# Optimization experiments

Hardware: AMD Instinct MI355X
Metric: run time of the kernel (lower is better)

## Reference

```python
import jax, jax.numpy as jnp
import numpy as np

N_NODES = 100000
N_EDGES = 3200000
EPS = 1e-5


def spmm(row, col, vals, h, n):
    # out[i] = sum_{e: row[e]==i} vals[e] * h[col[e]]  -- sparse A @ h in COO form
    return jax.ops.segment_sum(vals[:, None] * h[col], row, num_segments=n)


def batchnorm(h, gamma, beta):
    # BatchNorm1d in training mode: biased batch statistics over the node dim
    mean = jnp.mean(h, axis=0)
    var = jnp.mean((h - mean) ** 2, axis=0)
    return (h - mean) * jax.lax.rsqrt(var + EPS) * gamma + beta


def setup_inputs() -> dict:
    key = jax.random.key(0)
    ks = jax.random.split(key, 8)
    x = jax.random.normal(ks[0], (N_NODES, 256), dtype=jnp.float32)
    vals = jax.random.uniform(ks[1], (N_EDGES,), dtype=jnp.float32)
    row = jax.random.randint(ks[2], (N_EDGES,), 0, N_NODES, dtype=jnp.int32)
    col = jax.random.randint(ks[3], (N_EDGES,), 0, N_NODES, dtype=jnp.int32)
    W0 = jax.random.normal(ks[4], (256, 256), dtype=jnp.float32) * 0.05
    W1 = jax.random.normal(ks[5], (256, 256), dtype=jnp.float32) * 0.05
    W2 = jax.random.normal(ks[6], (256, 128), dtype=jnp.float32) * 0.05
    b0 = jnp.zeros((256,), jnp.float32)
    b1 = jnp.zeros((256,), jnp.float32)
    b2 = jnp.zeros((128,), jnp.float32)
    g0 = jnp.ones((256,), jnp.float32)
    g1 = jnp.ones((256,), jnp.float32)
    be0 = jnp.zeros((256,), jnp.float32)
    be1 = jnp.zeros((256,), jnp.float32)
    return {"x": x, "vals": vals, "W0": W0, "b0": b0, "g0": g0, "be0": be0,
            "W1": W1, "b1": b1, "g1": g1, "be1": be1, "W2": W2, "b2": b2,
            "row": row, "col": col}


def reference(x, vals, W0, b0, g0, be0, W1, b1, g1, be1, W2, b2, row, col):
    n = x.shape[0]
    # layer 0: linear -> SpMM -> BN -> ReLU (dropout is identity in eval)
    h = spmm(row, col, vals, x @ W0 + b0, n)
    h = jax.nn.relu(batchnorm(h, g0, be0))
    # layer 1
    h = spmm(row, col, vals, h @ W1 + b1, n)
    h = jax.nn.relu(batchnorm(h, g1, be1))
    # final projection
    h = spmm(row, col, vals, h @ W2 + b2, n)
    return h
```

## Files before the change

### kernel.cpp

```cpp
#include <hip/hip_runtime.h>


typedef __attribute__((ext_vector_type(8))) short s8b;
typedef __attribute__((ext_vector_type(4))) float f32x4;

__device__ inline unsigned short bf16_rne(float f) {
    unsigned u = __float_as_uint(f);
    return (unsigned short)((u + 0x7fffu + ((u >> 16) & 1u)) >> 16);
}
__device__ inline float bf16_to_f(unsigned short h) {
    return __uint_as_float((unsigned)h << 16);
}

#define NBLK_AC 256

__global__ __launch_bounds__(256) void bucket_hist(const int* __restrict__ row,
                                                   int* __restrict__ hist2d,
                                                   int E, int NB) {
    __shared__ int cnt[256];
    int t = threadIdx.x, blk = blockIdx.x;
    cnt[t] = 0;
    __syncthreads();
    int chunk = (E + gridDim.x - 1) / gridDim.x;
    int e0 = blk * chunk, e1 = min(E, e0 + chunk);
    for (int e = e0 + t; e < e1; e += 256) atomicAdd(&cnt[((unsigned)row[e]) >> 9], 1);
    __syncthreads();
    if (t < NB) hist2d[t * NBLK_AC + blk] = cnt[t];
}

__global__ __launch_bounds__(1024) void excl_scan(const int* __restrict__ in,
                                                  int* __restrict__ out, int L) {
    __shared__ int wsum[16];
    __shared__ int s_run;
    int t = threadIdx.x;
    int wid = t >> 6, lane = t & 63;
    if (t == 0) s_run = 0;
    __syncthreads();
    const int CHUNK = 1024 * 8;
    for (int base = 0; base < L; base += CHUNK) {
        int v[8];
        int local = 0;
        int i0 = base + t * 8;
#pragma unroll
        for (int j = 0; j < 8; ++j) {
            int idx = i0 + j;
            v[j] = (idx < L) ? in[idx] : 0;
            local += v[j];
        }
        int x = local;
#pragma unroll
        for (int off = 1; off < 64; off <<= 1) {
            int y = __shfl_up(x, off);
            if (lane >= off) x += y;
        }
        if (lane == 63) wsum[wid] = x;
        __syncthreads();
        if (wid == 0) {
            int w = (lane < 16) ? wsum[lane] : 0;
#pragma unroll
            for (int off = 1; off < 16; off <<= 1) {
                int y = __shfl_up(w, off);
                if (lane >= off) w += y;
            }
            if (lane < 16) wsum[lane] = w;
        }
        __syncthreads();
        int wave_off = (wid > 0) ? wsum[wid - 1] : 0;
        int chunk_total = wsum[15];
        int acc = (x - local) + wave_off + s_run;
#pragma unroll
        for (int j = 0; j < 8; ++j) {
            int idx = i0 + j;
            if (idx < L) out[idx] = acc;
            acc += v[j];
        }
        __syncthreads();
        if (t == 0) s_run += chunk_total;
        __syncthreads();
    }
}

__global__ __launch_bounds__(256) void bucket_scatter(const int* __restrict__ row,
                                                      const int* __restrict__ col,
                                                      const float* __restrict__ vals,
                                                      const int* __restrict__ base2d,
                                                      int2* __restrict__ ebuf,
                                                      int E, int NB) {
    __shared__ int cur[256];
    int t = threadIdx.x, blk = blockIdx.x;
    if (t < NB) cur[t] = base2d[t * NBLK_AC + blk];
    __syncthreads();
    int chunk = (E + gridDim.x - 1) / gridDim.x;
    int e0 = blk * chunk, e1 = min(E, e0 + chunk);
    for (int e = e0 + t; e < e1; e += 256) {
        int r = row[e];
        int b = ((unsigned)r) >> 9;
        int p = atomicAdd(&cur[b], 1);
        ebuf[p] = make_int2(((r & 511) << 23) | col[e], __float_as_int(vals[e]));
    }
}

__global__ __launch_bounds__(256) void bucket_sort(const int2* __restrict__ ebuf,
                                                   const int* __restrict__ base2d,
                                                   int2* __restrict__ edges,
                                                   int* __restrict__ rowptr,
                                                   int E, int M, int NB) {
    __shared__ int cnt[512];
    __shared__ int excl[512];
    int b = blockIdx.x, t = threadIdx.x;
    int bstart = base2d[b * NBLK_AC];
    int bend = (b + 1 < NB) ? base2d[(b + 1) * NBLK_AC] : E;
    cnt[t] = 0;
    cnt[t + 256] = 0;
    __syncthreads();
    for (int i = bstart + t; i < bend; i += 256)
        atomicAdd(&cnt[((unsigned)ebuf[i].x) >> 23], 1);
    __syncthreads();
    if (t == 0) {
        int a = 0;
#pragma unroll 8
        for (int i = 0; i < 512; ++i) { excl[i] = a; a += cnt[i]; }
    }
    __syncthreads();
    for (int rl = t; rl < 512; rl += 256) {
        int r0 = b * 512 + rl;
        if (r0 < M) rowptr[r0] = bstart + excl[rl];
    }
    if (b == 0 && t == 0) rowptr[M] = E;
    cnt[t] = excl[t];
    cnt[t + 256] = excl[t + 256];
    __syncthreads();
    for (int i = bstart + t; i < bend; i += 256) {
        int2 eb = ebuf[i];
        int rl = ((unsigned)eb.x) >> 23;
        int p = bstart + atomicAdd(&cnt[rl], 1);
        edges[p] = make_int2(eb.x & 0x7FFFFF, eb.y);
    }
}

__global__ void wsplit_kernel(const float* __restrict__ W, short* __restrict__ Wt_hi,
                              short* __restrict__ Wt_lo, int N) {
    const int K = 256;
    int i = blockIdx.x * blockDim.x + threadIdx.x;
    if (i >= K * N) return;
    int k = i / N, n = i % N;
    float f = W[i];
    unsigned short h = bf16_rne(f);
    unsigned short l = bf16_rne(f - bf16_to_f(h));
    Wt_hi[(size_t)n * K + k] = (short)h;
    Wt_lo[(size_t)n * K + k] = (short)l;
}

template <bool FIRST>
__global__ __launch_bounds__(256) void gemm_mfma_kernel(
    const void* __restrict__ Aptr, const short* __restrict__ Wth,
    const short* __restrict__ Wtl, const float* __restrict__ bias,
    const float* __restrict__ scale, const float* __restrict__ shift,
    unsigned short* __restrict__ C, int M, int N) {
    const int K = 256;
    const int LDT = 40;
    __shared__ short Ah[128 * LDT], Bh[128 * LDT], Bl[128 * LDT];

    int t = threadIdx.x;
    int wave = t >> 6, lane = t & 63;
    int wm = wave >> 1, wn = wave & 1;
    int row0 = blockIdx.x * 128;
    int n0 = blockIdx.y * 128;

    int srow = t >> 1;
    int skh = (t & 1) * 16;

    int lr = lane & 15;
    int lg = (lane >> 4) * 8;

    f32x4 acc[4][4];
#pragma unroll
    for (int i = 0; i < 4; ++i)
#pragma unroll
        for (int j = 0; j < 4; ++j) acc[i][j] = (f32x4){0.f, 0.f, 0.f, 0.f};

    for (int k0 = 0; k0 < K; k0 += 32) {
        float va[16];
        int gr = row0 + srow;
        if constexpr (FIRST) {
            if (gr < M) {
                const float4* ap = (const float4*)((const float*)Aptr + (size_t)gr * K + k0 + skh);
#pragma unroll
                for (int q = 0; q < 4; ++q) {
                    float4 v = ap[q];
                    va[4 * q + 0] = v.x; va[4 * q + 1] = v.y;
                    va[4 * q + 2] = v.z; va[4 * q + 3] = v.w;
                }
            } else {
#pragma unroll
                for (int q = 0; q < 16; ++q) va[q] = 0.f;
            }
        } else {
            if (gr < M) {
                const s8b* ap = (const s8b*)((const unsigned short*)Aptr + (size_t)gr * K + k0 + skh);
                s8b r0 = ap[0], r1 = ap[1];
#pragma unroll
                for (int q = 0; q < 8; ++q) {
                    va[q] = bf16_to_f((unsigned short)r0[q]);
                    va[8 + q] = bf16_to_f((unsigned short)r1[q]);
                }
            } else {
#pragma unroll
                for (int q = 0; q < 16; ++q) va[q] = 0.f;
            }
#pragma unroll
            for (int q = 0; q < 4; ++q) {
                float4 sc = *(const float4*)(scale + k0 + skh + 4 * q);
                float4 sh = *(const float4*)(shift + k0 + skh + 4 * q);
                va[4 * q + 0] = fmaxf(va[4 * q + 0] * sc.x + sh.x, 0.f);
                va[4 * q + 1] = fmaxf(va[4 * q + 1] * sc.y + sh.y, 0.f);
                va[4 * q + 2] = fmaxf(va[4 * q + 2] * sc.z + sh.z, 0.f);
                va[4 * q + 3] = fmaxf(va[4 * q + 3] * sc.w + sh.w, 0.f);
            }
        }
        s8b vh0, vh1;
#pragma unroll
        for (int q = 0; q < 8; ++q) {
            vh0[q] = (short)bf16_rne(va[q]);
            vh1[q] = (short)bf16_rne(va[8 + q]);
        }
        *(s8b*)&Ah[srow * LDT + skh]     = vh0;
        *(s8b*)&Ah[srow * LDT + skh + 8] = vh1;

        int gn = n0 + srow;
        const s8b* wph = (const s8b*)(Wth + (size_t)gn * K + k0 + skh);
        const s8b* wpl = (const s8b*)(Wtl + (size_t)gn * K + k0 + skh);
        s8b wh0 = wph[0], wh1 = wph[1];
        s8b wl0 = wpl[0], wl1 = wpl[1];
        *(s8b*)&Bh[srow * LDT + skh]     = wh0;
        *(s8b*)&Bh[srow * LDT + skh + 8] = wh1;
        *(s8b*)&Bl[srow * LDT + skh]     = wl0;
        *(s8b*)&Bl[srow * LDT + skh + 8] = wl1;
        __syncthreads();

        s8b a[4], bh[4], bl[4];
#pragma unroll
        for (int i = 0; i < 4; ++i)
            a[i] = *(const s8b*)&Ah[(wm * 64 + i * 16 + lr) * LDT + lg];
#pragma unroll
        for (int j = 0; j < 4; ++j) {
            int c = (wn * 64 + j * 16 + lr) * LDT + lg;
            bh[j] = *(const s8b*)&Bh[c];
            bl[j] = *(const s8b*)&Bl[c];
        }
#pragma unroll
        for (int i = 0; i < 4; ++i)
#pragma unroll
            for (int j = 0; j < 4; ++j) {
                acc[i][j] = __builtin_amdgcn_mfma_f32_16x16x32_bf16(a[i], bh[j], acc[i][j], 0, 0, 0);
                acc[i][j] = __builtin_amdgcn_mfma_f32_16x16x32_bf16(a[i], bl[j], acc[i][j], 0, 0, 0);
            }
        __syncthreads();
    }

    int lq = lane >> 4;
#pragma unroll
    for (int j = 0; j < 4; ++j) {
        int colg = n0 + wn * 64 + j * 16 + lr;
        float bb = bias[colg];
#pragma unroll
        for (int i = 0; i < 4; ++i) {
#pragma unroll
            for (int r = 0; r < 4; ++r) {
                int rowg = row0 + wm * 64 + i * 16 + lq * 4 + r;
                if (rowg < M) C[(size_t)rowg * N + colg] = bf16_rne(acc[i][j][r] + bb);
            }
        }
    }
}

template <int F, bool OUT_BF16>
__global__ __launch_bounds__(256) void spmm_kernel(const int* __restrict__ rowptr,
                                                   const int2* __restrict__ edges,
                                                   const unsigned short* __restrict__ H,
                                                   void* __restrict__ out, int M) {
    int wid = threadIdx.x >> 6;
    int lane = threadIdx.x & 63;
    int r = blockIdx.x * 4 + wid;
    if (r >= M) return;
    int e0 = rowptr[r], e1 = rowptr[r + 1];
    if constexpr (F == 256) {
        const ushort4* Hv = (const ushort4*)H;
        float4 acc = {0.f, 0.f, 0.f, 0.f};
        int e = e0;
        for (; e + 4 <= e1; e += 4) {
            int2 E0 = edges[e], E1 = edges[e + 1], E2 = edges[e + 2], E3 = edges[e + 3];
            ushort4 h0 = Hv[(size_t)E0.x * 64 + lane];
            ushort4 h1 = Hv[(size_t)E1.x * 64 + lane];
            ushort4 h2 = Hv[(size_t)E2.x * 64 + lane];
            ushort4 h3 = Hv[(size_t)E3.x * 64 + lane];
            float v0 = __int_as_float(E0.y), v1 = __int_as_float(E1.y);
            float v2 = __int_as_float(E2.y), v3 = __int_as_float(E3.y);
            acc.x += v0 * bf16_to_f(h0.x); acc.y += v0 * bf16_to_f(h0.y);
            acc.z += v0 * bf16_to_f(h0.z); acc.w += v0 * bf16_to_f(h0.w);
            acc.x += v1 * bf16_to_f(h1.x); acc.y += v1 * bf16_to_f(h1.y);
            acc.z += v1 * bf16_to_f(h1.z); acc.w += v1 * bf16_to_f(h1.w);
            acc.x += v2 * bf16_to_f(h2.x); acc.y += v2 * bf16_to_f(h2.y);
            acc.z += v2 * bf16_to_f(h2.z); acc.w += v2 * bf16_to_f(h2.w);
            acc.x += v3 * bf16_to_f(h3.x); acc.y += v3 * bf16_to_f(h3.y);
            acc.z += v3 * bf16_to_f(h3.z); acc.w += v3 * bf16_to_f(h3.w);
        }
        for (; e < e1; ++e) {
            int2 E0 = edges[e];
            ushort4 h0 = Hv[(size_t)E0.x * 64 + lane];
            float v0 = __int_as_float(E0.y);
            acc.x += v0 * bf16_to_f(h0.x); acc.y += v0 * bf16_to_f(h0.y);
            acc.z += v0 * bf16_to_f(h0.z); acc.w += v0 * bf16_to_f(h0.w);
        }
        if constexpr (OUT_BF16) {
            ushort4 o;
            o.x = bf16_rne(acc.x); o.y = bf16_rne(acc.y);
            o.z = bf16_rne(acc.z); o.w = bf16_rne(acc.w);
            ((ushort4*)out)[(size_t)r * 64 + lane] = o;
        } else {
            ((float4*)out)[(size_t)r * 64 + lane] = acc;
        }
    } else {
        const ushort2* Hv = (const ushort2*)H;
        float2 acc = {0.f, 0.f};
        int e = e0;
        for (; e + 4 <= e1; e += 4) {
            int2 E0 = edges[e], E1 = edges[e + 1], E2 = edges[e + 2], E3 = edges[e + 3];
            ushort2 h0 = Hv[(size_t)E0.x * 64 + lane];
            ushort2 h1 = Hv[(size_t)E1.x * 64 + lane];
            ushort2 h2 = Hv[(size_t)E2.x * 64 + lane];
            ushort2 h3 = Hv[(size_t)E3.x * 64 + lane];
            float v0 = __int_as_float(E0.y), v1 = __int_as_float(E1.y);
            float v2 = __int_as_float(E2.y), v3 = __int_as_float(E3.y);
            acc.x += v0 * bf16_to_f(h0.x); acc.y += v0 * bf16_to_f(h0.y);
            acc.x += v1 * bf16_to_f(h1.x); acc.y += v1 * bf16_to_f(h1.y);
            acc.x += v2 * bf16_to_f(h2.x); acc.y += v2 * bf16_to_f(h2.y);
            acc.x += v3 * bf16_to_f(h3.x); acc.y += v3 * bf16_to_f(h3.y);
        }
        for (; e < e1; ++e) {
            int2 E0 = edges[e];
            ushort2 h0 = Hv[(size_t)E0.x * 64 + lane];
            float v0 = __int_as_float(E0.y);
            acc.x += v0 * bf16_to_f(h0.x); acc.y += v0 * bf16_to_f(h0.y);
        }
        if constexpr (OUT_BF16) {
            ushort2 o;
            o.x = bf16_rne(acc.x); o.y = bf16_rne(acc.y);
            ((ushort2*)out)[(size_t)r * 64 + lane] = o;
        } else {
            ((float2*)out)[(size_t)r * 64 + lane] = acc;
        }
    }
}

__global__ __launch_bounds__(256) void bn_stats_kernel(const unsigned short* __restrict__ H,
                                                       float* __restrict__ sums,
                                                       float* __restrict__ sumsq, int M) {
    int c = threadIdx.x;
    int nb = gridDim.x;
    int rows_per = (M + nb - 1) / nb;
    int r0 = blockIdx.x * rows_per;
    int r1 = min(M, r0 + rows_per);
    float s = 0.f, q = 0.f;
    for (int r = r0; r < r1; ++r) {
        float v = bf16_to_f(H[(size_t)r * 256 + c]);
        s += v;
        q += v * v;
    }
    atomicAdd(&sums[c], s);
    atomicAdd(&sumsq[c], q);
}

__global__ void bn_finalize_kernel(const float* __restrict__ sums, const float* __restrict__ sumsq,
                                   const float* __restrict__ g, const float* __restrict__ be,
                                   float* __restrict__ scale, float* __restrict__ shift, int M) {
    int c = threadIdx.x;
    float mean = sums[c] / (float)M;
    float var = sumsq[c] / (float)M - mean * mean;
    float inv = rsqrtf(var + 1e-5f);
    float s = g[c] * inv;
    scale[c] = s;
    shift[c] = be[c] - mean * s;
}

extern "C" void kernel_launch(void* const* d_in, const int* in_sizes, int n_in,
                              void* d_out, int out_size, void* d_ws, size_t ws_size,
                              hipStream_t stream) {
    const float* x   = (const float*)d_in[0];
    const float* vals= (const float*)d_in[1];
    const float* W0  = (const float*)d_in[2];
    const float* b0  = (const float*)d_in[3];
    const float* g0  = (const float*)d_in[4];
    const float* be0 = (const float*)d_in[5];
    const float* W1  = (const float*)d_in[6];
    const float* b1  = (const float*)d_in[7];
    const float* g1  = (const float*)d_in[8];
    const float* be1 = (const float*)d_in[9];
    const float* W2  = (const float*)d_in[10];
    const float* b2  = (const float*)d_in[11];
    const int* row   = (const int*)d_in[12];
    const int* col   = (const int*)d_in[13];
    const int E = in_sizes[1];
    const int M = in_sizes[0] / 256;
    float* out = (float*)d_out;

    char* ws = (char*)d_ws;
    size_t off = 0;
    auto alloc = [&](size_t bytes) -> void* {
        void* p = ws + off;
        off += (bytes + 255) & ~(size_t)255;
        return p;
    };
    unsigned short* hA = (unsigned short*)alloc((size_t)M * 256 * 2);
    unsigned short* hB = (unsigned short*)alloc((size_t)M * 256 * 2);
    int2*  edges = (int2*)alloc((size_t)E * 8);
    int2*  ebuf  = (int2*)alloc((size_t)E * 8);
    int*   rowptr= (int*)alloc((size_t)(M + 1) * 4);
    float* sums  = (float*)alloc(256 * 4);
    float* sumsq = (float*)alloc(256 * 4);
    float* scale = (float*)alloc(256 * 4);
    float* shift = (float*)alloc(256 * 4);
    short* Wth   = (short*)alloc((size_t)256 * 256 * 2);
    short* Wtl   = (short*)alloc((size_t)256 * 256 * 2);
    const int NB = (M + 511) >> 9;
    int* hist2d = (int*)alloc((size_t)NB * NBLK_AC * 4);
    int* base2d = (int*)alloc((size_t)NB * NBLK_AC * 4);

    bucket_hist<<<NBLK_AC, 256, 0, stream>>>(row, hist2d, E, NB);
    excl_scan<<<1, 1024, 0, stream>>>(hist2d, base2d, NB * NBLK_AC);
    bucket_scatter<<<NBLK_AC, 256, 0, stream>>>(row, col, vals, base2d, ebuf, E, NB);
    bucket_sort<<<NB, 256, 0, stream>>>(ebuf, base2d, edges, rowptr, E, M, NB);

    int gx = (M + 127) / 128;
    int spmm_grid = (M + 3) / 4;

    wsplit_kernel<<<(256 * 256 + 255) / 256, 256, 0, stream>>>(W0, Wth, Wtl, 256);
    gemm_mfma_kernel<true><<<dim3(gx, 2), 256, 0, stream>>>(x, Wth, Wtl, b0, nullptr, nullptr, hA, M, 256);
    spmm_kernel<256, true><<<spmm_grid, 256, 0, stream>>>(rowptr, edges, hA, hB, M);

    hipMemsetAsync(sums, 0, 2048, stream);
    bn_stats_kernel<<<256, 256, 0, stream>>>(hB, sums, sumsq, M);
    bn_finalize_kernel<<<1, 256, 0, stream>>>(sums, sumsq, g0, be0, scale, shift, M);

    wsplit_kernel<<<(256 * 256 + 255) / 256, 256, 0, stream>>>(W1, Wth, Wtl, 256);
    gemm_mfma_kernel<false><<<dim3(gx, 2), 256, 0, stream>>>(hB, Wth, Wtl, b1, scale, shift, hA, M, 256);
    spmm_kernel<256, true><<<spmm_grid, 256, 0, stream>>>(rowptr, edges, hA, hB, M);

    hipMemsetAsync(sums, 0, 2048, stream);
    bn_stats_kernel<<<256, 256, 0, stream>>>(hB, sums, sumsq, M);
    bn_finalize_kernel<<<1, 256, 0, stream>>>(sums, sumsq, g1, be1, scale, shift, M);

    wsplit_kernel<<<(256 * 128 + 255) / 256, 256, 0, stream>>>(W2, Wth, Wtl, 128);
    gemm_mfma_kernel<false><<<dim3(gx, 1), 256, 0, stream>>>(hB, Wth, Wtl, b2, scale, shift, hA, M, 128);
    spmm_kernel<128, false><<<spmm_grid, 256, 0, stream>>>(rowptr, edges, hA, out, M);
}
```

Baseline: 1.321 ms.

## Drop LDS staging in GEMM; load MFMA fragments directly and unfuse BN-ReLU

The GEMM no longer stages A and W tiles through shared memory with barriers. Each wave now loads its MFMA operand fragments straight from global memory, converting fp32 input to bf16 in registers. The BatchNorm scale/shift plus ReLU that was fused into the GEMM A-load moves to a separate elementwise kernel writing a new bf16 buffer. This removes LDS traffic and syncs, but adds redundant global loads across waves and an extra read/write pass over the activation per layer.

```diff
diff --git a/kernel.cpp b/kernel.cpp
--- a/kernel.cpp
+++ b/kernel.cpp
@@ -151,25 +151,44 @@
     Wt_lo[(size_t)n * K + k] = (short)l;
 }
 
+__global__ __launch_bounds__(256) void act_kernel(const unsigned short* __restrict__ hB,
+                                                  const float* __restrict__ scale,
+                                                  const float* __restrict__ shift,
+                                                  unsigned short* __restrict__ hC,
+                                                  int n8) {
+    int i = blockIdx.x * blockDim.x + threadIdx.x;
+    int stride = gridDim.x * blockDim.x;
+    for (; i < n8; i += stride) {
+        int kb = (i & 31) * 8;
+        s8b h = ((const s8b*)hB)[i];
+        float4 s0 = *(const float4*)(scale + kb);
+        float4 s1 = *(const float4*)(scale + kb + 4);
+        float4 t0 = *(const float4*)(shift + kb);
+        float4 t1 = *(const float4*)(shift + kb + 4);
+        s8b o;
+        o[0] = (short)bf16_rne(fmaxf(bf16_to_f((unsigned short)h[0]) * s0.x + t0.x, 0.f));
+        o[1] = (short)bf16_rne(fmaxf(bf16_to_f((unsigned short)h[1]) * s0.y + t0.y, 0.f));
+        o[2] = (short)bf16_rne(fmaxf(bf16_to_f((unsigned short)h[2]) * s0.z + t0.z, 0.f));
+        o[3] = (short)bf16_rne(fmaxf(bf16_to_f((unsigned short)h[3]) * s0.w + t0.w, 0.f));
+        o[4] = (short)bf16_rne(fmaxf(bf16_to_f((unsigned short)h[4]) * s1.x + t1.x, 0.f));
+        o[5] = (short)bf16_rne(fmaxf(bf16_to_f((unsigned short)h[5]) * s1.y + t1.y, 0.f));
+        o[6] = (short)bf16_rne(fmaxf(bf16_to_f((unsigned short)h[6]) * s1.z + t1.z, 0.f));
+        o[7] = (short)bf16_rne(fmaxf(bf16_to_f((unsigned short)h[7]) * s1.w + t1.w, 0.f));
+        ((s8b*)hC)[i] = o;
+    }
+}
+
 template <bool FIRST>
-__global__ __launch_bounds__(256) void gemm_mfma_kernel(
+__global__ __launch_bounds__(256) void gemm_direct(
     const void* __restrict__ Aptr, const short* __restrict__ Wth,
     const short* __restrict__ Wtl, const float* __restrict__ bias,
-    const float* __restrict__ scale, const float* __restrict__ shift,
     unsigned short* __restrict__ C, int M, int N) {
     const int K = 256;
-    const int LDT = 40;
-    __shared__ short Ah[128 * LDT], Bh[128 * LDT], Bl[128 * LDT];
-
     int t = threadIdx.x;
     int wave = t >> 6, lane = t & 63;
     int wm = wave >> 1, wn = wave & 1;
     int row0 = blockIdx.x * 128;
     int n0 = blockIdx.y * 128;
-
-    int srow = t >> 1;
-    int skh = (t & 1) * 16;
-
     int lr = lane & 15;
     int lg = (lane >> 4) * 8;
 
@@ -180,73 +199,32 @@
         for (int j = 0; j < 4; ++j) acc[i][j] = (f32x4){0.f, 0.f, 0.f, 0.f};
 
     for (int k0 = 0; k0 < K; k0 += 32) {
-        float va[16];
-        int gr = row0 + srow;
-        if constexpr (FIRST) {
-            if (gr < M) {
-                const float4* ap = (const float4*)((const float*)Aptr + (size_t)gr * K + k0 + skh);
-#pragma unroll
-                for (int q = 0; q < 4; ++q) {
-                    float4 v = ap[q];
-                    va[4 * q + 0] = v.x; va[4 * q + 1] = v.y;
-                    va[4 * q + 2] = v.z; va[4 * q + 3] = v.w;
+        s8b a[4], bh[4], bl[4];
+#pragma unroll
+        for (int i = 0; i < 4; ++i) {
+            int gr = row0 + wm * 64 + i * 16 + lr;
+            if constexpr (FIRST) {
+                if (gr < M) {
+                    const float4* xp = (const float4*)((const float*)Aptr + (size_t)gr * K + k0 + lg);
+                    float4 v0 = xp[0], v1 = xp[1];
+                    a[i][0] = (short)bf16_rne(v0.x); a[i][1] = (short)bf16_rne(v0.y);
+                    a[i][2] = (short)bf16_rne(v0.z); a[i][3] = (short)bf16_rne(v0.w);
+                    a[i][4] = (short)bf16_rne(v1.x); a[i][5] = (short)bf16_rne(v1.y);
+                    a[i][6] = (short)bf16_rne(v1.z); a[i][7] = (short)bf16_rne(v1.w);
+                } else {
+                    a[i] = (s8b){0, 0, 0, 0, 0, 0, 0, 0};
                 }
             } else {
-#pragma unroll
-                for (int q = 0; q < 16; ++q) va[q] = 0.f;
+                a[i] = (gr < M)
+                    ? *(const s8b*)((const unsigned short*)Aptr + (size_t)gr * K + k0 + lg)
+                    : (s8b){0, 0, 0, 0, 0, 0, 0, 0};
             }
-        } else {
-            if (gr < M) {
-                const s8b* ap = (const s8b*)((const unsigned short*)Aptr + (size_t)gr * K + k0 + skh);
-                s8b r0 = ap[0], r1 = ap[1];
-#pragma unroll
-                for (int q = 0; q < 8; ++q) {
-                    va[q] = bf16_to_f((unsigned short)r0[q]);
-                    va[8 + q] = bf16_to_f((unsigned short)r1[q]);
-                }
-            } else {
-#pragma unroll
-                for (int q = 0; q < 16; ++q) va[q] = 0.f;
-            }
-#pragma unroll
-            for (int q = 0; q < 4; ++q) {
-                float4 sc = *(const float4*)(scale + k0 + skh + 4 * q);
-                float4 sh = *(const float4*)(shift + k0 + skh + 4 * q);
-                va[4 * q + 0] = fmaxf(va[4 * q + 0] * sc.x + sh.x, 0.f);
-                va[4 * q + 1] = fmaxf(va[4 * q + 1] * sc.y + sh.y, 0.f);
-                va[4 * q + 2] = fmaxf(va[4 * q + 2] * sc.z + sh.z, 0.f);
-                va[4 * q + 3] = fmaxf(va[4 * q + 3] * sc.w + sh.w, 0.f);
-            }
-        }
-        s8b vh0, vh1;
-#pragma unroll
-        for (int q = 0; q < 8; ++q) {
-            vh0[q] = (short)bf16_rne(va[q]);
-            vh1[q] = (short)bf16_rne(va[8 + q]);
-        }
-        *(s8b*)&Ah[srow * LDT + skh]     = vh0;
-        *(s8b*)&Ah[srow * LDT + skh + 8] = vh1;
-
-        int gn = n0 + srow;
-        const s8b* wph = (const s8b*)(Wth + (size_t)gn * K + k0 + skh);
-        const s8b* wpl = (const s8b*)(Wtl + (size_t)gn * K + k0 + skh);
-        s8b wh0 = wph[0], wh1 = wph[1];
-        s8b wl0 = wpl[0], wl1 = wpl[1];
-        *(s8b*)&Bh[srow * LDT + skh]     = wh0;
-        *(s8b*)&Bh[srow * LDT + skh + 8] = wh1;
-        *(s8b*)&Bl[srow * LDT + skh]     = wl0;
-        *(s8b*)&Bl[srow * LDT + skh + 8] = wl1;
-        __syncthreads();
-
-        s8b a[4], bh[4], bl[4];
-#pragma unroll
-        for (int i = 0; i < 4; ++i)
-            a[i] = *(const s8b*)&Ah[(wm * 64 + i * 16 + lr) * LDT + lg];
+        }
 #pragma unroll
         for (int j = 0; j < 4; ++j) {
-            int c = (wn * 64 + j * 16 + lr) * LDT + lg;
-            bh[j] = *(const s8b*)&Bh[c];
-            bl[j] = *(const s8b*)&Bl[c];
+            int gn = n0 + wn * 64 + j * 16 + lr;
+            bh[j] = *(const s8b*)(Wth + (size_t)gn * K + k0 + lg);
+            bl[j] = *(const s8b*)(Wtl + (size_t)gn * K + k0 + lg);
         }
 #pragma unroll
         for (int i = 0; i < 4; ++i)
@@ -255,7 +233,6 @@
                 acc[i][j] = __builtin_amdgcn_mfma_f32_16x16x32_bf16(a[i], bh[j], acc[i][j], 0, 0, 0);
                 acc[i][j] = __builtin_amdgcn_mfma_f32_16x16x32_bf16(a[i], bl[j], acc[i][j], 0, 0, 0);
             }
-        __syncthreads();
     }
 
     int lq = lane >> 4;
@@ -413,6 +390,7 @@
     };
     unsigned short* hA = (unsigned short*)alloc((size_t)M * 256 * 2);
     unsigned short* hB = (unsigned short*)alloc((size_t)M * 256 * 2);
+    unsigned short* hC = (unsigned short*)alloc((size_t)M * 256 * 2);
     int2*  edges = (int2*)alloc((size_t)E * 8);
     int2*  ebuf  = (int2*)alloc((size_t)E * 8);
     int*   rowptr= (int*)alloc((size_t)(M + 1) * 4);
@@ -433,24 +411,27 @@
 
     int gx = (M + 127) / 128;
     int spmm_grid = (M + 3) / 4;
+    int n8 = M * 32;
 
     wsplit_kernel<<<(256 * 256 + 255) / 256, 256, 0, stream>>>(W0, Wth, Wtl, 256);
-    gemm_mfma_kernel<true><<<dim3(gx, 2), 256, 0, stream>>>(x, Wth, Wtl, b0, nullptr, nullptr, hA, M, 256);
+    gemm_direct<true><<<dim3(gx, 2), 256, 0, stream>>>(x, Wth, Wtl, b0, hA, M, 256);
     spmm_kernel<256, true><<<spmm_grid, 256, 0, stream>>>(rowptr, edges, hA, hB, M);
 
     hipMemsetAsync(sums, 0, 2048, stream);
     bn_stats_kernel<<<256, 256, 0, stream>>>(hB, sums, sumsq, M);
     bn_finalize_kernel<<<1, 256, 0, stream>>>(sums, sumsq, g0, be0, scale, shift, M);
 
+    act_kernel<<<2048, 256, 0, stream>>>(hB, scale, shift, hC, n8);
     wsplit_kernel<<<(256 * 256 + 255) / 256, 256, 0, stream>>>(W1, Wth, Wtl, 256);
-    gemm_mfma_kernel<false><<<dim3(gx, 2), 256, 0, stream>>>(hB, Wth, Wtl, b1, scale, shift, hA, M, 256);
+    gemm_direct<false><<<dim3(gx, 2), 256, 0, stream>>>(hC, Wth, Wtl, b1, hA, M, 256);
     spmm_kernel<256, true><<<spmm_grid, 256, 0, stream>>>(rowptr, edges, hA, hB, M);
 
     hipMemsetAsync(sums, 0, 2048, stream);
     bn_stats_kernel<<<256, 256, 0, stream>>>(hB, sums, sumsq, M);
     bn_finalize_kernel<<<1, 256, 0, stream>>>(sums, sumsq, g1, be1, scale, shift, M);
 
+    act_kernel<<<2048, 256, 0, stream>>>(hB, scale, shift, hC, n8);
     wsplit_kernel<<<(256 * 128 + 255) / 256, 256, 0, stream>>>(W2, Wth, Wtl, 128);
-    gemm_mfma_kernel<false><<<dim3(gx, 1), 256, 0, stream>>>(hB, Wth, Wtl, b2, scale, shift, hA, M, 128);
+    gemm_direct<false><<<dim3(gx, 1), 256, 0, stream>>>(hC, Wth, Wtl, b2, hA, M, 128);
     spmm_kernel<128, false><<<spmm_grid, 256, 0, stream>>>(rowptr, edges, hA, out, M);
 }
```

After: 1.496 ms. +13.3%, slower.
